# Optimization experiments

Hardware: AMD Instinct MI355X
Metric: run time of the kernel (lower is better)

## Reference

```python
import jax, jax.numpy as jnp
import numpy as np

B, S, H = 4, 4096, 1024
NUM_LEVELS, DECAY = 3, 0.8
D0, D1 = 512, 204  # int(1024*0.5), int(512*0.5*0.8)


def _xavier(key, shape):
    fan_in, fan_out = shape
    return jax.random.normal(key, shape, dtype=jnp.float32) * np.sqrt(2.0 / (fan_in + fan_out))


def setup_inputs() -> dict:
    key = jax.random.key(0)
    ks = jax.random.split(key, 8)
    return {
        "keys": jax.random.normal(ks[0], (B, S, H), dtype=jnp.float32),
        "values": jax.random.normal(ks[1], (B, S, H), dtype=jnp.float32),
        "importance": jax.random.uniform(ks[2], (B, S), dtype=jnp.float32),
        # encoder layers (stored as [in, out]; torch Linear applies x @ W.T + b)
        "We0": _xavier(ks[3], (H, D0)), "be0": jnp.zeros((D0,), jnp.float32),
        "We1": _xavier(ks[4], (D0, D1)), "be1": jnp.zeros((D1,), jnp.float32),
        # decoder layers
        "Wd0": _xavier(ks[5], (D0, H)), "bd0": jnp.zeros((H,), jnp.float32),
        "Wd1": _xavier(ks[6], (D1, D0)), "bd1": jnp.zeros((D0,), jnp.float32),
    }


def _level_sizes(n):
    sizes, remaining = [], n
    for i in range(NUM_LEVELS):
        if i == NUM_LEVELS - 1:
            sizes.append(remaining)
        else:
            sz = int(remaining * (1 - DECAY) * DECAY ** i)
            sizes.append(sz)
            remaining -= sz
    return sizes


def reference(keys, values, importance, We0, be0, We1, be1, Wd0, bd0, Wd1, bd1):
    n = B * S
    fk = keys.reshape(n, H)
    fv = values.reshape(n, H)
    sorted_idx = jnp.argsort(-importance.reshape(-1))  # descending importance
    sizes = _level_sizes(n)

    def chain(x, level):
        # encode 0..level-1 with ReLU, then decode level-1..0 with ReLU
        if level >= 1:
            x = jax.nn.relu(x @ We0 + be0)
        if level >= 2:
            x = jax.nn.relu(x @ We1 + be1)
            x = jax.nn.relu(x @ Wd1 + bd1)
        if level >= 1:
            x = jax.nn.relu(x @ Wd0 + bd0)
        return x

    ck = jnp.zeros_like(fk)
    cv = jnp.zeros_like(fv)
    start = 0
    for level, size in enumerate(sizes):
        if size <= 0:
            continue
        idx = jax.lax.dynamic_slice(sorted_idx, (start,), (size,))
        ck = ck.at[idx].set(chain(fk[idx], level))
        cv = cv.at[idx].set(chain(fv[idx], level))
        start += size
    return ck.reshape(B, S, H), cv.reshape(B, S, H)
```

## Files before the change

### kernel.cpp

```cpp
#include <hip/hip_runtime.h>

typedef __attribute__((ext_vector_type(8))) short short8;
typedef __attribute__((ext_vector_type(4))) float f32x4;

#define N_TOK   16384
#define HDIM    1024
#define OUT_OFF 16777216
#define M1ROWS  26216
#define M2ROWS  22022
#define L2ROW0  4194

__device__ __forceinline__ unsigned short f2bf(float f) {
  unsigned int u = __float_as_uint(f);
  u += 0x7FFFu + ((u >> 16) & 1u);
  return (unsigned short)(u >> 16);
}

__device__ __forceinline__ void rowmap(int r, int& is_v, int& rank) {
  if (r < 2097)       { is_v = 0; rank = 3276 + r; }
  else if (r < 4194)  { is_v = 1; rank = 1179 + r; }
  else if (r < 15205) { is_v = 0; rank = 1179 + r; }
  else                { is_v = 1; rank = r - 9832; }
}

__global__ __launch_bounds__(256) void rank_count(const float* __restrict__ imp,
                                                  int* __restrict__ counts) {
  __shared__ float sj[2048];
  const int i = blockIdx.x * 256 + threadIdx.x;
  const int jbase = blockIdx.y * 2048;
  const float vi = imp[i];
  for (int s = threadIdx.x; s < 2048; s += 256) sj[s] = imp[jbase + s];
  __syncthreads();
  int cnt = 0;
  #pragma unroll 8
  for (int s = 0; s < 2048; ++s) {
    float vj = sj[s];
    bool gt = vj > vi;
    bool eq = (vj == vi) && ((jbase + s) < i);
    cnt += (gt || eq) ? 1 : 0;
  }
  atomicAdd(&counts[i], cnt);
}

__global__ __launch_bounds__(256) void scatter_order(const int* __restrict__ counts,
                                                     int* __restrict__ order) {
  int i = blockIdx.x * 256 + threadIdx.x;
  order[counts[i]] = i;
}

__global__ __launch_bounds__(256) void wconv(unsigned short* __restrict__ dst,
                                             const float* __restrict__ src,
                                             int Nd, int Kd, int Nsrc, int Ksrc) {
  int idx = blockIdx.x * 256 + threadIdx.x;
  if (idx >= Nd * Kd) return;
  int n = idx / Kd, k = idx % Kd;
  float v = (n < Nsrc && k < Ksrc) ? src[k * Nsrc + n] : 0.f;
  dst[idx] = f2bf(v);
}

__global__ __launch_bounds__(256) void gather_rows(unsigned short* __restrict__ X,
                                                   const float* __restrict__ keys,
                                                   const float* __restrict__ values,
                                                   const int* __restrict__ order) {
  int r = blockIdx.x;
  int is_v, rank; rowmap(r, is_v, rank);
  int token = order[rank];
  const float* src = (is_v ? values : keys) + (size_t)token * HDIM;
  int c = threadIdx.x * 4;
  float4 f = *reinterpret_cast<const float4*>(src + c);
  ushort4 h;
  h.x = f2bf(f.x); h.y = f2bf(f.y); h.z = f2bf(f.z); h.w = f2bf(f.w);
  *reinterpret_cast<ushort4*>(X + (size_t)r * HDIM + c) = h;
}

__global__ __launch_bounds__(256) void copy_level0(float* __restrict__ out,
                                                   const float* __restrict__ keys,
                                                   const float* __restrict__ values,
                                                   const int* __restrict__ order) {
  int b = blockIdx.x;
  int is_v = b & 1, rank = b >> 1;
  int token = order[rank];
  const float* src = (is_v ? values : keys) + (size_t)token * HDIM;
  float* dst = out + (is_v ? OUT_OFF : 0) + (size_t)token * HDIM;
  int c = threadIdx.x * 4;
  *reinterpret_cast<float4*>(dst + c) = *reinterpret_cast<const float4*>(src + c);
}

#define GLDS16(g, l) __builtin_amdgcn_global_load_lds( \
    (const __attribute__((address_space(1))) void*)(g), \
    (__attribute__((address_space(3))) void*)(l), 16, 0, 0)

template<int MODE>
__global__ __launch_bounds__(512) void gemm_bias_relu(
    const unsigned short* __restrict__ A, int M, int K,
    const unsigned short* __restrict__ Bt, int N,
    const float* __restrict__ bias, int Nbias,
    unsigned short* __restrict__ Cbf, int ldc,
    float* __restrict__ outf, const int* __restrict__ order,
    int NP, int NC) {
  __shared__ __align__(16) unsigned short S[3][12288];
  const int bid = blockIdx.x;
  const int r8 = bid & 7;
  const int rest = bid >> 3;
  const int c8 = rest % NC;
  const int q8 = rest / NC;
  const int p8 = q8 * 8 + r8;
  if (p8 >= NP) return;
  const int row0 = p8 * 256, col0 = c8 * 128;

  const int tid = threadIdx.x;
  const int wave = tid >> 6, lane = tid & 63;
  const int lrow = lane >> 2;
  const int lk = (((lane & 3) ^ ((lane >> 3) & 3)) << 3);
  const int wr = (wave >> 1) * 64, wc = (wave & 1) * 64;

  const unsigned short* gp[3];
  int ldso[3];
  #pragma unroll
  for (int j = 0; j < 3; ++j) {
    const int g = wave * 3 + j;
    const bool isA = g < 16;
    int rr = isA ? (row0 + g * 16 + lrow) : (col0 + (g - 16) * 16 + lrow);
    const int lim = isA ? M : N;
    if (rr >= lim) rr = 0;
    gp[j] = (isA ? A : Bt) + (size_t)rr * K + lk;
    ldso[j] = g * 512;
  }

  f32x4 acc[4][4] = {};
  const int fr = lane & 15;
  const int qoff = (((lane >> 4) ^ ((fr >> 1) & 3)) << 3);

  const int nt = K >> 5;
  #pragma unroll
  for (int j = 0; j < 3; ++j) GLDS16(gp[j], S[0] + ldso[j]);
  #pragma unroll
  for (int j = 0; j < 3; ++j) GLDS16(gp[j] + 32, S[1] + ldso[j]);

  int cur = 0;
  for (int t = 0; t < nt; ++t) {
    if (t + 1 < nt) asm volatile("s_waitcnt vmcnt(3)" ::: "memory");
    else            asm volatile("s_waitcnt vmcnt(0)" ::: "memory");
    __builtin_amdgcn_s_barrier();
    __builtin_amdgcn_sched_barrier(0);
    const unsigned short* as = S[cur];
    const unsigned short* bs = S[cur] + 8192;
    short8 af[4], bfv[4];
    #pragma unroll
    for (int m = 0; m < 4; ++m)
      af[m] = *reinterpret_cast<const short8*>(as + (wr + m * 16 + fr) * 32 + qoff);
    #pragma unroll
    for (int n = 0; n < 4; ++n)
      bfv[n] = *reinterpret_cast<const short8*>(bs + (wc + n * 16 + fr) * 32 + qoff);
    if (t + 2 < nt) {
      const int k2 = (t + 2) << 5;
      int nb = cur + 2; if (nb >= 3) nb -= 3;
      #pragma unroll
      for (int j = 0; j < 3; ++j) GLDS16(gp[j] + k2, S[nb] + ldso[j]);
    }
    #pragma unroll
    for (int m = 0; m < 4; ++m)
      #pragma unroll
      for (int n = 0; n < 4; ++n)
        acc[m][n] = __builtin_amdgcn_mfma_f32_16x16x32_bf16(af[m], bfv[n], acc[m][n], 0, 0, 0);
    cur = (cur == 2) ? 0 : cur + 1;
  }

  const int orow = (lane >> 4) * 4;
  const int ocol = lane & 15;
  if (MODE == 0) {
    #pragma unroll
    for (int m = 0; m < 4; ++m) {
      #pragma unroll
      for (int n = 0; n < 4; ++n) {
        #pragma unroll
        for (int j = 0; j < 4; ++j) {
          int r = row0 + wr + m * 16 + orow + j;
          int c = col0 + wc + n * 16 + ocol;
          if (r < M && c < N) {
            float v = acc[m][n][j] + (c < Nbias ? bias[c] : 0.f);
            Cbf[(size_t)r * ldc + c] = f2bf(fmaxf(v, 0.f));
          }
        }
      }
    }
  } else {
    float* Cl = (float*)S;
    #pragma unroll 1
    for (int p = 0; p < 4; ++p) {
      __builtin_amdgcn_s_barrier();
      if ((wave >> 1) == p) {
        #pragma unroll
        for (int m = 0; m < 4; ++m)
          #pragma unroll
          for (int n = 0; n < 4; ++n)
            #pragma unroll
            for (int j = 0; j < 4; ++j) {
              int rr = m * 16 + orow + j;
              int cc = wc + n * 16 + ocol;
              float v = acc[m][n][j] + bias[col0 + cc];
              Cl[rr * 136 + cc] = fmaxf(v, 0.f);
            }
      }
      __builtin_amdgcn_s_barrier();
      #pragma unroll
      for (int u = 0; u < 4; ++u) {
        int unit = tid + u * 512;
        int rr = unit >> 5, ch = unit & 31;
        int r = row0 + p * 64 + rr;
        if (r < M) {
          int iv, rk; rowmap(r, iv, rk);
          int token = order[rk];
          f32x4 v = *reinterpret_cast<const f32x4*>(Cl + rr * 136 + ch * 4);
          *reinterpret_cast<f32x4*>(outf + (size_t)(iv ? OUT_OFF : 0) +
                                    (size_t)token * HDIM + col0 + ch * 4) = v;
        }
      }
    }
  }
}

static inline int swz_grid(int NP, int NC) { return 8 * NC * ((NP + 7) / 8); }

extern "C" void kernel_launch(void* const* d_in, const int* in_sizes, int n_in,
                              void* d_out, int out_size, void* d_ws, size_t ws_size,
                              hipStream_t stream) {
  const float* keys   = (const float*)d_in[0];
  const float* values = (const float*)d_in[1];
  const float* imp    = (const float*)d_in[2];
  const float* We0    = (const float*)d_in[3];
  const float* be0    = (const float*)d_in[4];
  const float* We1    = (const float*)d_in[5];
  const float* be1    = (const float*)d_in[6];
  const float* Wd0    = (const float*)d_in[7];
  const float* bd0    = (const float*)d_in[8];
  const float* Wd1    = (const float*)d_in[9];
  const float* bd1    = (const float*)d_in[10];

  char* ws = (char*)d_ws;
  int* counts           = (int*)(ws);
  int* order            = (int*)(ws + 65536);
  unsigned short* We0T  = (unsigned short*)(ws + 131072);
  unsigned short* We1T  = (unsigned short*)(ws + 1179648);
  unsigned short* Wd1T  = (unsigned short*)(ws + 1409024);
  unsigned short* Wd0T  = (unsigned short*)(ws + 1638400);
  unsigned short* Y     = (unsigned short*)(ws + 2686976);
  unsigned short* Z     = (unsigned short*)(ws + 29532160);
  unsigned short* X     = (unsigned short*)(ws + 39398016);
  float* outf = (float*)d_out;

  hipMemsetAsync(counts, 0, 65536, stream);
  rank_count<<<dim3(64, 8), 256, 0, stream>>>(imp, counts);
  scatter_order<<<64, 256, 0, stream>>>(counts, order);

  wconv<<<2048, 256, 0, stream>>>(We0T, We0, 512, 1024, 512, 1024);
  wconv<<<448,  256, 0, stream>>>(We1T, We1, 224, 512, 204, 512);
  wconv<<<448,  256, 0, stream>>>(Wd1T, Wd1, 512, 224, 512, 204);
  wconv<<<2048, 256, 0, stream>>>(Wd0T, Wd0, 1024, 512, 1024, 512);

  gather_rows<<<M1ROWS, 256, 0, stream>>>(X, keys, values, order);
  copy_level0<<<6552, 256, 0, stream>>>(outf, keys, values, order);

  gemm_bias_relu<0><<<swz_grid(103, 4), 512, 0, stream>>>(
      X, M1ROWS, 1024, We0T, 512, be0, 512, Y, 512, nullptr, nullptr, 103, 4);

  gemm_bias_relu<0><<<swz_grid(87, 2), 512, 0, stream>>>(
      Y + (size_t)L2ROW0 * 512, M2ROWS, 512, We1T, 224, be1, 204, Z, 224,
      nullptr, nullptr, 87, 2);

  gemm_bias_relu<0><<<swz_grid(87, 4), 512, 0, stream>>>(
      Z, M2ROWS, 224, Wd1T, 512, bd1, 512, Y + (size_t)L2ROW0 * 512, 512,
      nullptr, nullptr, 87, 4);

  gemm_bias_relu<1><<<swz_grid(103, 8), 512, 0, stream>>>(
      Y, M1ROWS, 512, Wd0T, 1024, bd0, 1024, nullptr, 0, outf, order, 103, 8);
}
```

Baseline: 272.1 us.

## Restructure GEMM pipeline to three-stage prefetch with compile-time K and padded mid dim

The GEMM kernel becomes templated on K, so the loop trip count is a compile-time constant. The prefetch is reworked so all three LDS stages are filled up front, with a new load issued into the just-consumed buffer after each MFMA block. MFMA sections are wrapped in s_setprio, and the launch bounds now request 4 waves per SIMD. The bottleneck dimension is padded from 224 to 256 to match the 32-wide K tiles and the 128-wide N tiles, and the fp32 epilogue LDS stride changes from 136 to 132. The extra barrier per iteration and the occupancy hint may add register pressure or sync cost.

```diff
diff --git a/kernel.cpp b/kernel.cpp
--- a/kernel.cpp
+++ b/kernel.cpp
@@ -90,30 +90,31 @@
     (const __attribute__((address_space(1))) void*)(g), \
     (__attribute__((address_space(3))) void*)(l), 16, 0, 0)
 
-template<int MODE>
-__global__ __launch_bounds__(512) void gemm_bias_relu(
-    const unsigned short* __restrict__ A, int M, int K,
+template<int MODE, int K>
+__global__ __launch_bounds__(512, 4) void g2(
+    const unsigned short* __restrict__ A, int M,
     const unsigned short* __restrict__ Bt, int N,
     const float* __restrict__ bias, int Nbias,
     unsigned short* __restrict__ Cbf, int ldc,
     float* __restrict__ outf, const int* __restrict__ order,
     int NP, int NC) {
+  constexpr int NH = K / 32;
   __shared__ __align__(16) unsigned short S[3][12288];
+
   const int bid = blockIdx.x;
-  const int r8 = bid & 7;
-  const int rest = bid >> 3;
-  const int c8 = rest % NC;
-  const int q8 = rest / NC;
+  const int r8 = bid & 7, rest = bid >> 3;
+  const int c8 = rest % NC, q8 = rest / NC;
   const int p8 = q8 * 8 + r8;
   if (p8 >= NP) return;
   const int row0 = p8 * 256, col0 = c8 * 128;
 
   const int tid = threadIdx.x;
   const int wave = tid >> 6, lane = tid & 63;
+  const int wm = wave >> 1, wn = wave & 1;
+  const int fr = lane & 15, lch = lane >> 4;
+
   const int lrow = lane >> 2;
-  const int lk = (((lane & 3) ^ ((lane >> 3) & 3)) << 3);
-  const int wr = (wave >> 1) * 64, wc = (wave & 1) * 64;
-
+  const int sswz = (((lane & 3) ^ ((lane >> 3) & 3)) << 3);
   const unsigned short* gp[3];
   int ldso[3];
   #pragma unroll
@@ -123,51 +124,60 @@
     int rr = isA ? (row0 + g * 16 + lrow) : (col0 + (g - 16) * 16 + lrow);
     const int lim = isA ? M : N;
     if (rr >= lim) rr = 0;
-    gp[j] = (isA ? A : Bt) + (size_t)rr * K + lk;
+    gp[j] = (isA ? A : Bt) + (size_t)rr * K + sswz;
     ldso[j] = g * 512;
   }
 
+  const int qoff = ((lch ^ ((fr >> 1) & 3)) << 3);
+  const int abase = (wm * 64 + fr) * 32 + qoff;
+  const int bbase = 8192 + (wn * 64 + fr) * 32 + qoff;
+
   f32x4 acc[4][4] = {};
-  const int fr = lane & 15;
-  const int qoff = (((lane >> 4) ^ ((fr >> 1) & 3)) << 3);
-
-  const int nt = K >> 5;
+
   #pragma unroll
-  for (int j = 0; j < 3; ++j) GLDS16(gp[j], S[0] + ldso[j]);
-  #pragma unroll
-  for (int j = 0; j < 3; ++j) GLDS16(gp[j] + 32, S[1] + ldso[j]);
+  for (int h = 0; h < 3; ++h)
+    #pragma unroll
+    for (int j = 0; j < 3; ++j)
+      GLDS16(gp[j] + h * 32, S[h] + ldso[j]);
+  asm volatile("s_waitcnt vmcnt(6)" ::: "memory");
+  __builtin_amdgcn_s_barrier();
 
   int cur = 0;
-  for (int t = 0; t < nt; ++t) {
-    if (t + 1 < nt) asm volatile("s_waitcnt vmcnt(3)" ::: "memory");
-    else            asm volatile("s_waitcnt vmcnt(0)" ::: "memory");
+  #pragma unroll 1
+  for (int h = 0; h < NH; ++h) {
+    const unsigned short* sl = S[cur];
+    short8 a[4], b[4];
+    #pragma unroll
+    for (int m = 0; m < 4; ++m)
+      a[m] = *reinterpret_cast<const short8*>(sl + abase + m * 512);
+    #pragma unroll
+    for (int n = 0; n < 4; ++n)
+      b[n] = *reinterpret_cast<const short8*>(sl + bbase + n * 512);
+    asm volatile("s_waitcnt lgkmcnt(0)" ::: "memory");
+    __builtin_amdgcn_sched_barrier(0);
     __builtin_amdgcn_s_barrier();
-    __builtin_amdgcn_sched_barrier(0);
-    const unsigned short* as = S[cur];
-    const unsigned short* bs = S[cur] + 8192;
-    short8 af[4], bfv[4];
+    __builtin_amdgcn_s_setprio(1);
     #pragma unroll
     for (int m = 0; m < 4; ++m)
-      af[m] = *reinterpret_cast<const short8*>(as + (wr + m * 16 + fr) * 32 + qoff);
-    #pragma unroll
-    for (int n = 0; n < 4; ++n)
-      bfv[n] = *reinterpret_cast<const short8*>(bs + (wc + n * 16 + fr) * 32 + qoff);
-    if (t + 2 < nt) {
-      const int k2 = (t + 2) << 5;
-      int nb = cur + 2; if (nb >= 3) nb -= 3;
-      #pragma unroll
-      for (int j = 0; j < 3; ++j) GLDS16(gp[j] + k2, S[nb] + ldso[j]);
+      #pragma unroll
+      for (int n = 0; n < 4; ++n)
+        acc[m][n] = __builtin_amdgcn_mfma_f32_16x16x32_bf16(a[m], b[n], acc[m][n], 0, 0, 0);
+    __builtin_amdgcn_s_setprio(0);
+    if (h + 3 < NH) {
+      const int kc = (h + 3) * 32;
+      #pragma unroll
+      for (int j = 0; j < 3; ++j) GLDS16(gp[j] + kc, S[cur] + ldso[j]);
+      asm volatile("s_waitcnt vmcnt(6)" ::: "memory");
+    } else if (h + 2 < NH) {
+      asm volatile("s_waitcnt vmcnt(3)" ::: "memory");
+    } else if (h + 1 < NH) {
+      asm volatile("s_waitcnt vmcnt(0)" ::: "memory");
     }
-    #pragma unroll
-    for (int m = 0; m < 4; ++m)
-      #pragma unroll
-      for (int n = 0; n < 4; ++n)
-        acc[m][n] = __builtin_amdgcn_mfma_f32_16x16x32_bf16(af[m], bfv[n], acc[m][n], 0, 0, 0);
+    __builtin_amdgcn_s_barrier();
     cur = (cur == 2) ? 0 : cur + 1;
   }
 
-  const int orow = (lane >> 4) * 4;
-  const int ocol = lane & 15;
+  const int orow = lch * 4;
   if (MODE == 0) {
     #pragma unroll
     for (int m = 0; m < 4; ++m) {
@@ -175,8 +185,8 @@
       for (int n = 0; n < 4; ++n) {
         #pragma unroll
         for (int j = 0; j < 4; ++j) {
-          int r = row0 + wr + m * 16 + orow + j;
-          int c = col0 + wc + n * 16 + ocol;
+          int r = row0 + wm * 64 + m * 16 + orow + j;
+          int c = col0 + wn * 64 + n * 16 + fr;
           if (r < M && c < N) {
             float v = acc[m][n][j] + (c < Nbias ? bias[c] : 0.f);
             Cbf[(size_t)r * ldc + c] = f2bf(fmaxf(v, 0.f));
@@ -189,7 +199,7 @@
     #pragma unroll 1
     for (int p = 0; p < 4; ++p) {
       __builtin_amdgcn_s_barrier();
-      if ((wave >> 1) == p) {
+      if (wm == p) {
         #pragma unroll
         for (int m = 0; m < 4; ++m)
           #pragma unroll
@@ -197,9 +207,9 @@
             #pragma unroll
             for (int j = 0; j < 4; ++j) {
               int rr = m * 16 + orow + j;
-              int cc = wc + n * 16 + ocol;
+              int cc = wn * 64 + n * 16 + fr;
               float v = acc[m][n][j] + bias[col0 + cc];
-              Cl[rr * 136 + cc] = fmaxf(v, 0.f);
+              Cl[rr * 132 + cc] = fmaxf(v, 0.f);
             }
       }
       __builtin_amdgcn_s_barrier();
@@ -211,7 +221,7 @@
         if (r < M) {
           int iv, rk; rowmap(r, iv, rk);
           int token = order[rk];
-          f32x4 v = *reinterpret_cast<const f32x4*>(Cl + rr * 136 + ch * 4);
+          f32x4 v = *reinterpret_cast<const f32x4*>(Cl + rr * 132 + ch * 4);
           *reinterpret_cast<f32x4*>(outf + (size_t)(iv ? OUT_OFF : 0) +
                                     (size_t)token * HDIM + col0 + ch * 4) = v;
         }
@@ -220,7 +230,7 @@
   }
 }
 
-static inline int swz_grid(int NP, int NC) { return 8 * NC * ((NP + 7) / 8); }
+static inline int swzg(int NP, int NC) { return 8 * NC * ((NP + 7) / 8); }
 
 extern "C" void kernel_launch(void* const* d_in, const int* in_sizes, int n_in,
                               void* d_out, int out_size, void* d_ws, size_t ws_size,
@@ -242,11 +252,11 @@
   int* order            = (int*)(ws + 65536);
   unsigned short* We0T  = (unsigned short*)(ws + 131072);
   unsigned short* We1T  = (unsigned short*)(ws + 1179648);
-  unsigned short* Wd1T  = (unsigned short*)(ws + 1409024);
-  unsigned short* Wd0T  = (unsigned short*)(ws + 1638400);
-  unsigned short* Y     = (unsigned short*)(ws + 2686976);
-  unsigned short* Z     = (unsigned short*)(ws + 29532160);
-  unsigned short* X     = (unsigned short*)(ws + 39398016);
+  unsigned short* Wd1T  = (unsigned short*)(ws + 1441792);
+  unsigned short* Wd0T  = (unsigned short*)(ws + 1703936);
+  unsigned short* Y     = (unsigned short*)(ws + 2752512);
+  unsigned short* Z     = (unsigned short*)(ws + 29597696);
+  unsigned short* X     = (unsigned short*)(ws + 40872960);
   float* outf = (float*)d_out;
 
   hipMemsetAsync(counts, 0, 65536, stream);
@@ -254,24 +264,24 @@
   scatter_order<<<64, 256, 0, stream>>>(counts, order);
 
   wconv<<<2048, 256, 0, stream>>>(We0T, We0, 512, 1024, 512, 1024);
-  wconv<<<448,  256, 0, stream>>>(We1T, We1, 224, 512, 204, 512);
-  wconv<<<448,  256, 0, stream>>>(Wd1T, Wd1, 512, 224, 512, 204);
+  wconv<<<512,  256, 0, stream>>>(We1T, We1, 256, 512, 204, 512);
+  wconv<<<512,  256, 0, stream>>>(Wd1T, Wd1, 512, 256, 512, 204);
   wconv<<<2048, 256, 0, stream>>>(Wd0T, Wd0, 1024, 512, 1024, 512);
 
   gather_rows<<<M1ROWS, 256, 0, stream>>>(X, keys, values, order);
   copy_level0<<<6552, 256, 0, stream>>>(outf, keys, values, order);
 
-  gemm_bias_relu<0><<<swz_grid(103, 4), 512, 0, stream>>>(
-      X, M1ROWS, 1024, We0T, 512, be0, 512, Y, 512, nullptr, nullptr, 103, 4);
-
-  gemm_bias_relu<0><<<swz_grid(87, 2), 512, 0, stream>>>(
-      Y + (size_t)L2ROW0 * 512, M2ROWS, 512, We1T, 224, be1, 204, Z, 224,
+  g2<0, 1024><<<swzg(103, 4), 512, 0, stream>>>(
+      X, M1ROWS, We0T, 512, be0, 512, Y, 512, nullptr, nullptr, 103, 4);
+
+  g2<0, 512><<<swzg(87, 2), 512, 0, stream>>>(
+      Y + (size_t)L2ROW0 * 512, M2ROWS, We1T, 256, be1, 204, Z, 256,
       nullptr, nullptr, 87, 2);
 
-  gemm_bias_relu<0><<<swz_grid(87, 4), 512, 0, stream>>>(
-      Z, M2ROWS, 224, Wd1T, 512, bd1, 512, Y + (size_t)L2ROW0 * 512, 512,
+  g2<0, 256><<<swzg(87, 4), 512, 0, stream>>>(
+      Z, M2ROWS, Wd1T, 512, bd1, 512, Y + (size_t)L2ROW0 * 512, 512,
       nullptr, nullptr, 87, 4);
 
-  gemm_bias_relu<1><<<swz_grid(103, 8), 512, 0, stream>>>(
-      Y, M1ROWS, 512, Wd0T, 1024, bd0, 1024, nullptr, 0, outf, order, 103, 8);
-}
+  g2<1, 512><<<swzg(103, 8), 512, 0, stream>>>(
+      Y, M1ROWS, Wd0T, 1024, bd0, 1024, nullptr, 0, outf, order, 103, 8);
+}
```

Result: no change. 276.6 us (+1.6%).
